# Kernel optimization log

Measured on AMD Instinct MI355X. Metric: run time of the kernel, lower is better.

Reference implementation:

```python
import jax, jax.numpy as jnp
import numpy as np

N_NODES = 100000
D = 64


def sage_conv(x, src, dst, W_l, b_l, W_r, n_nodes):
    """PyG SAGEConv with mean aggregation and root_weight=True:
    out_i = lin_l(mean_{j in N(i)} x_j) + lin_r(x_i)
    Aggregation happens on raw features (as in PyG), then linear transforms.
    """
    deg = jax.ops.segment_sum(jnp.ones_like(dst, dtype=x.dtype), dst, num_segments=n_nodes)
    aggr = jax.ops.segment_sum(x[src], dst, num_segments=n_nodes)  # [N, D] gather-scatter
    aggr = aggr / jnp.maximum(deg, 1.0)[:, None]                    # mean (0 for isolated nodes)
    return aggr @ W_l.T + b_l + x @ W_r.T


def setup_inputs() -> dict:
    key = jax.random.key(0)
    k_x, k_e, k1, k2, k3, k4 = jax.random.split(key, 6)
    x = jax.random.normal(k_x, (N_NODES, D), dtype=jnp.float32)
    edge_index = jax.random.randint(k_e, (2, 1600000), 0, N_NODES, dtype=jnp.int64)
    s = 1.0 / np.sqrt(D)
    # layer 1 (SAGEConv: lin_l has bias, lin_r has no bias)
    W1_l = jax.random.uniform(k1, (D, D), jnp.float32, -s, s)
    b1_l = jnp.zeros((D,), jnp.float32)
    W1_r = jax.random.uniform(k2, (D, D), jnp.float32, -s, s)
    # layer 2
    W2_l = jax.random.uniform(k3, (D, D), jnp.float32, -s, s)
    b2_l = jnp.zeros((D,), jnp.float32)
    W2_r = jax.random.uniform(k4, (D, D), jnp.float32, -s, s)
    return {"x": x, "edge_index": edge_index,
            "W1_l": W1_l, "b1_l": b1_l, "W1_r": W1_r,
            "W2_l": W2_l, "b2_l": b2_l, "W2_r": W2_r}


def reference(x, edge_index, W1_l, b1_l, W1_r, W2_l, b2_l, W2_r):
    src, dst = edge_index[0], edge_index[1]
    n = x.shape[0]
    x1 = sage_conv(x, src, dst, W1_l, b1_l, W1_r, n)
    x2 = sage_conv(x1, src, dst, W2_l, b2_l, W2_r, n)
    return x2
```

## Files before the change

kernel.cpp:

```cpp
#include <hip/hip_runtime.h>

#define DD 64
#define DTILE 128
#define BSHIFT 7
#define NBUCK_MAX 800
#define SEGCAP 4096

typedef unsigned short ushort_t;

static __device__ __forceinline__ unsigned short f2bf(float f)
{
    unsigned u = __float_as_uint(f);
    unsigned r = (u + 0x7FFFu + ((u >> 16) & 1u)) >> 16;
    return (unsigned short)r;
}
static __device__ __forceinline__ float bf_lo(unsigned w) { return __uint_as_float(w << 16); }
static __device__ __forceinline__ float bf_hi(unsigned w) { return __uint_as_float(w & 0xFFFF0000u); }


__global__ __launch_bounds__(256)
void bucket_count(const int* __restrict__ dst, int* __restrict__ partialCnt,
                  int nE, int chunk, int nbuck)
{
    __shared__ int bins[NBUCK_MAX];
    int blk = blockIdx.x, t = threadIdx.x;
    for (int i = t; i < nbuck; i += 256) bins[i] = 0;
    __syncthreads();
    int e0 = blk * chunk;
    int e1 = e0 + chunk; if (e1 > nE) e1 = nE;
    for (int e = e0 + t; e < e1; e += 256)
        atomicAdd(&bins[dst[e] >> BSHIFT], 1);
    __syncthreads();
    for (int i = t; i < nbuck; i += 256)
        partialCnt[(size_t)i * 256 + blk] = bins[i];
}

__global__ __launch_bounds__(256)
void bucket_scanblocks(int* __restrict__ partialCnt, int* __restrict__ bucketTot)
{
    __shared__ int s[256];
    int b = blockIdx.x, t = threadIdx.x;
    int v = partialCnt[(size_t)b * 256 + t];
    s[t] = v;
    __syncthreads();
    for (int off = 1; off < 256; off <<= 1) {
        int u = (t >= off) ? s[t - off] : 0;
        __syncthreads();
        s[t] += u;
        __syncthreads();
    }
    partialCnt[(size_t)b * 256 + t] = s[t] - v;
    if (t == 255) bucketTot[b] = s[255];
}

__global__ __launch_bounds__(1024)
void bucket_scanbase(const int* __restrict__ bucketTot, int* __restrict__ bucketBase,
                     int* __restrict__ rs, int nbuck, int nN)
{
    __shared__ int s[1024];
    int t = threadIdx.x;
    int v = (t < nbuck) ? bucketTot[t] : 0;
    s[t] = v;
    __syncthreads();
    for (int off = 1; off < 1024; off <<= 1) {
        int u = (t >= off) ? s[t - off] : 0;
        __syncthreads();
        s[t] += u;
        __syncthreads();
    }
    if (t < nbuck) bucketBase[t] = s[t] - v;
    if (t == nbuck - 1) {
        bucketBase[nbuck] = s[t];
        rs[nN] = s[t];
    }
}

__global__ __launch_bounds__(256)
void bucket_scatter(const int* __restrict__ src, const int* __restrict__ dst,
                    const int* __restrict__ partialCnt,
                    const int* __restrict__ bucketBase,
                    int* __restrict__ buckEdges, int nE, int chunk, int nbuck)
{
    __shared__ int bins[NBUCK_MAX];
    __shared__ int wOff[NBUCK_MAX];
    int blk = blockIdx.x, t = threadIdx.x;
    for (int i = t; i < nbuck; i += 256) {
        bins[i] = 0;
        wOff[i] = bucketBase[i] + partialCnt[(size_t)i * 256 + blk];
    }
    __syncthreads();
    int e0 = blk * chunk;
    int e1 = e0 + chunk; if (e1 > nE) e1 = nE;
    for (int e = e0 + t; e < e1; e += 256) {
        int d = dst[e];
        int sv = src[e];
        int bb = d >> BSHIFT;
        int r = atomicAdd(&bins[bb], 1);
        buckEdges[wOff[bb] + r] = sv | ((d & 127) << 17);
    }
}

__global__ __launch_bounds__(256)
void bucket_finalize(const int* __restrict__ buckEdges,
                     const int* __restrict__ bucketBase,
                     int* __restrict__ rs, int* __restrict__ csr,
                     int nN)
{
    __shared__ int eLds[SEGCAP];
    __shared__ int segLds[SEGCAP];
    __shared__ int deg[128];
    __shared__ int basec[128];
    __shared__ int cur[128];
    int b = blockIdx.x, t = threadIdx.x;
    int e0 = bucketBase[b], e1 = bucketBase[b + 1];
    int nb = e1 - e0;
    bool staged = (nb <= SEGCAP);
    if (t < 128) deg[t] = 0;
    __syncthreads();
    for (int i = t; i < nb; i += 256) {
        int p = buckEdges[e0 + i];
        if (staged) eLds[i] = p;
        atomicAdd(&deg[(p >> 17) & 127], 1);
    }
    __syncthreads();
    if (t < 128) basec[t] = deg[t];
    __syncthreads();
    for (int off = 1; off < 128; off <<= 1) {
        int u = 0;
        if (t < 128 && t >= off) u = basec[t - off];
        __syncthreads();
        if (t < 128) basec[t] += u;
        __syncthreads();
    }
    int nodeBase = b << BSHIFT;
    if (t < 128) {
        int node = nodeBase + t;
        int ex = basec[t] - deg[t];
        if (node < nN) rs[node] = e0 + ex;
        cur[t] = ex;
    }
    __syncthreads();
    for (int i = t; i < nb; i += 256) {
        int p = staged ? eLds[i] : buckEdges[e0 + i];
        int dl = (p >> 17) & 127;
        int slot = atomicAdd(&cur[dl], 1);
        int sv = p & 0x1FFFF;
        if (staged) segLds[slot] = sv;
        else        csr[e0 + slot] = sv;
    }
    __syncthreads();
    if (staged)
        for (int i = t; i < nb; i += 256)
            csr[e0 + i] = segLds[i];
}

__global__ __launch_bounds__(256)
void tobf16_kernel(const float* __restrict__ in, ushort_t* __restrict__ outh,
                   int nTot8)
{
    int i = blockIdx.x * 256 + threadIdx.x;
    if (i >= nTot8) return;
    float4 v0 = *(const float4*)(in + (size_t)i * 8);
    float4 v1 = *(const float4*)(in + (size_t)i * 8 + 4);
    uint4 o;
    o.x = (unsigned)f2bf(v0.x) | ((unsigned)f2bf(v0.y) << 16);
    o.y = (unsigned)f2bf(v0.z) | ((unsigned)f2bf(v0.w) << 16);
    o.z = (unsigned)f2bf(v1.x) | ((unsigned)f2bf(v1.y) << 16);
    o.w = (unsigned)f2bf(v1.z) | ((unsigned)f2bf(v1.w) << 16);
    *(uint4*)(outh + (size_t)i * 8) = o;
}

__global__ void prep_kernel(const float* __restrict__ W1l,
                            const float* __restrict__ W1r,
                            const float* __restrict__ W2l,
                            const float* __restrict__ W2r,
                            const float* __restrict__ b1,
                            const float* __restrict__ b2,
                            float* __restrict__ MT1, float* __restrict__ MT2,
                            float* __restrict__ MT3, float* __restrict__ c0,
                            float* __restrict__ c1)
{
    int f = blockIdx.x;
    int k = threadIdx.x;
    float m1 = 0.f, m2 = 0.f, m3 = 0.f;
    for (int j = 0; j < DD; ++j) {
        float a2l = W2l[f * DD + j];
        float a2r = W2r[f * DD + j];
        float w1l = W1l[j * DD + k];
        float w1r = W1r[j * DD + k];
        m1 = fmaf(a2l, w1l, m1);
        m2 = fmaf(a2l, w1r, m2);
        m2 = fmaf(a2r, w1l, m2);
        m3 = fmaf(a2r, w1r, m3);
    }
    MT1[k * DD + f] = m1;
    MT2[k * DD + f] = m2;
    MT3[k * DD + f] = m3;
    float t1 = W2l[f * DD + k] * b1[k];
    float t0 = W2r[f * DD + k] * b1[k];
    for (int off = 1; off < 64; off <<= 1) {
        t1 += __shfl_xor(t1, off);
        t0 += __shfl_xor(t0, off);
    }
    if (k == 0) {
        c1[f] = t1;
        c0[f] = t0 + b2[f];
    }
}

__global__ __launch_bounds__(256, 4)
void aggregate_bf16g(const ushort_t* __restrict__ xh,
                     const int* __restrict__ csr,
                     const int* __restrict__ rs,
                     ushort_t* __restrict__ aggrh, int nN)
{
    int lane = threadIdx.x & 63;
    int w = threadIdx.x >> 6;
    int g  = lane >> 3;
    int gl = lane & 7;
    int node = (blockIdx.x * 4 + w) * 8 + g;
    int valid = node < nN;
    int nd = valid ? node : nN - 1;
    int beg = rs[nd], end = rs[nd + 1];
    int deg = end - beg;

    float4 aL0 = {0,0,0,0}, aH0 = {0,0,0,0};
    float4 aL1 = {0,0,0,0}, aH1 = {0,0,0,0};
    float4 aL2 = {0,0,0,0}, aH2 = {0,0,0,0};
    float4 aL3 = {0,0,0,0}, aH3 = {0,0,0,0};

#define ROWA(S, L, H)                                                         \
    {                                                                         \
        uint4 v = *(const uint4*)(xh + (size_t)(S) * DD + gl * 8);            \
        L.x += bf_lo(v.x); L.y += bf_hi(v.x);                                 \
        L.z += bf_lo(v.y); L.w += bf_hi(v.y);                                 \
        H.x += bf_lo(v.z); H.y += bf_hi(v.z);                                 \
        H.z += bf_lo(v.w); H.w += bf_hi(v.w);                                 \
    }
#define ROWM(S, MM, L, H)                                                     \
    {                                                                         \
        uint4 v = *(const uint4*)(xh + (size_t)(S) * DD + gl * 8);            \
        L.x = fmaf(MM, bf_lo(v.x), L.x); L.y = fmaf(MM, bf_hi(v.x), L.y);     \
        L.z = fmaf(MM, bf_lo(v.y), L.z); L.w = fmaf(MM, bf_hi(v.y), L.w);     \
        H.x = fmaf(MM, bf_lo(v.z), H.x); H.y = fmaf(MM, bf_hi(v.z), H.y);     \
        H.z = fmaf(MM, bf_lo(v.w), H.z); H.w = fmaf(MM, bf_hi(v.w), H.w);     \
    }

    for (int ch = 0; ch < deg; ch += 8) {
        int ii = ch + gl;
        int myIdx = csr[(ii < deg) ? (beg + ii) : beg];
        int lb = g << 3;
        if (ch + 8 <= deg) {
            int s0 = __shfl(myIdx, lb + 0);
            int s1 = __shfl(myIdx, lb + 1);
            int s2 = __shfl(myIdx, lb + 2);
            int s3 = __shfl(myIdx, lb + 3);
            ROWA(s0, aL0, aH0) ROWA(s1, aL1, aH1)
            ROWA(s2, aL2, aH2) ROWA(s3, aL3, aH3)
            int s4 = __shfl(myIdx, lb + 4);
            int s5 = __shfl(myIdx, lb + 5);
            int s6 = __shfl(myIdx, lb + 6);
            int s7 = __shfl(myIdx, lb + 7);
            ROWA(s4, aL0, aH0) ROWA(s5, aL1, aH1)
            ROWA(s6, aL2, aH2) ROWA(s7, aL3, aH3)
        } else {
            int rem = deg - ch;
            int s0 = __shfl(myIdx, lb + 0);
            int s1 = __shfl(myIdx, lb + 1);
            int s2 = __shfl(myIdx, lb + 2);
            int s3 = __shfl(myIdx, lb + 3);
            float m0 = (0 < rem) ? 1.f : 0.f;
            float m1 = (1 < rem) ? 1.f : 0.f;
            float m2 = (2 < rem) ? 1.f : 0.f;
            float m3 = (3 < rem) ? 1.f : 0.f;
            ROWM(s0, m0, aL0, aH0) ROWM(s1, m1, aL1, aH1)
            ROWM(s2, m2, aL2, aH2) ROWM(s3, m3, aL3, aH3)
            int s4 = __shfl(myIdx, lb + 4);
            int s5 = __shfl(myIdx, lb + 5);
            int s6 = __shfl(myIdx, lb + 6);
            int s7 = __shfl(myIdx, lb + 7);
            float m4 = (4 < rem) ? 1.f : 0.f;
            float m5 = (5 < rem) ? 1.f : 0.f;
            float m6 = (6 < rem) ? 1.f : 0.f;
            float m7 = (7 < rem) ? 1.f : 0.f;
            ROWM(s4, m4, aL0, aH0) ROWM(s5, m5, aL1, aH1)
            ROWM(s6, m6, aL2, aH2) ROWM(s7, m7, aL3, aH3)
        }
    }
#undef ROWA
#undef ROWM

    float4 L, H;
    L.x = (aL0.x + aL1.x) + (aL2.x + aL3.x);
    L.y = (aL0.y + aL1.y) + (aL2.y + aL3.y);
    L.z = (aL0.z + aL1.z) + (aL2.z + aL3.z);
    L.w = (aL0.w + aL1.w) + (aL2.w + aL3.w);
    H.x = (aH0.x + aH1.x) + (aH2.x + aH3.x);
    H.y = (aH0.y + aH1.y) + (aH2.y + aH3.y);
    H.z = (aH0.z + aH1.z) + (aH2.z + aH3.z);
    H.w = (aH0.w + aH1.w) + (aH2.w + aH3.w);
    if (valid) {
        float inv = 1.0f / (float)(deg > 0 ? deg : 1);
        uint4 o;
        o.x = (unsigned)f2bf(L.x * inv) | ((unsigned)f2bf(L.y * inv) << 16);
        o.y = (unsigned)f2bf(L.z * inv) | ((unsigned)f2bf(L.w * inv) << 16);
        o.z = (unsigned)f2bf(H.x * inv) | ((unsigned)f2bf(H.y * inv) << 16);
        o.w = (unsigned)f2bf(H.z * inv) | ((unsigned)f2bf(H.w * inv) << 16);
        *(uint4*)(aggrh + (size_t)node * DD + gl * 8) = o;
    }
}

__global__ __launch_bounds__(512)
void tri_dense6(const ushort_t* __restrict__ agg2h,
                const ushort_t* __restrict__ agg1h,
                const ushort_t* __restrict__ xh,
                const float* __restrict__ MT1,
                const float* __restrict__ MT2,
                const float* __restrict__ MT3,
                const float* __restrict__ c0,
                const float* __restrict__ c1,
                const int* __restrict__ rs,
                float* __restrict__ out, int nN)
{
    __shared__ float t_lds[DTILE * 65];
    int tid = threadIdx.x;
    int nl  = tid & 127;
    int fbase = __builtin_amdgcn_readfirstlane((tid >> 7) * 16);
    int base = blockIdx.x * DTILE;
    int node = base + nl;
    int gn = node < nN ? node : nN - 1;

    float ind = (rs[gn + 1] - rs[gn]) > 0 ? 1.0f : 0.0f;
    float acc[16];
#pragma unroll
    for (int j = 0; j < 16; ++j)
        acc[j] = fmaf(ind, c1[fbase + j], c0[fbase + j]);

#define STAGE(SRCH)                                                           \
    {                                                                         \
        _Pragma("unroll")                                                     \
        for (int i = 0; i < 2; ++i) {                                         \
            int fi = i * 512 + tid;                  \
            int row = fi >> 3;                                                \
            int col = (fi & 7) * 8;                                           \
            int grow = base + row;                                            \
            if (grow >= nN) grow = nN - 1;                                    \
            uint4 v = *(const uint4*)((SRCH) + (size_t)grow * DD + col);      \
            float4 lo, hi;                                                    \
            lo.x = bf_lo(v.x); lo.y = bf_hi(v.x);                             \
            lo.z = bf_lo(v.y); lo.w = bf_hi(v.y);                             \
            hi.x = bf_lo(v.z); hi.y = bf_hi(v.z);                             \
            hi.z = bf_lo(v.w); hi.w = bf_hi(v.w);                             \
            *(float4*)&t_lds[row * 65 + col] = lo;                            \
            *(float4*)&t_lds[row * 65 + col + 4] = hi;                        \
        }                                                                     \
    }

#define PHASE(MT)                                                             \
    {                                                                         \
        _Pragma("unroll 1")                                                   \
        for (int k = 0; k < DD; k += 4) {                                     \
            float i0 = t_lds[nl * 65 + k + 0];                                \
            float i1 = t_lds[nl * 65 + k + 1];                                \
            float i2 = t_lds[nl * 65 + k + 2];                                \
            float i3 = t_lds[nl * 65 + k + 3];                                \
            const float* mr = (MT) + k * DD + fbase;                          \
            _Pragma("unroll")                                                 \
            for (int j = 0; j < 16; ++j) acc[j] = fmaf(i0, mr[j], acc[j]);    \
            _Pragma("unroll")                                                 \
            for (int j = 0; j < 16; ++j) acc[j] = fmaf(i1, mr[DD + j], acc[j]); \
            _Pragma("unroll")                                                 \
            for (int j = 0; j < 16; ++j) acc[j] = fmaf(i2, mr[2 * DD + j], acc[j]); \
            _Pragma("unroll")                                                 \
            for (int j = 0; j < 16; ++j) acc[j] = fmaf(i3, mr[3 * DD + j], acc[j]); \
        }                                                                     \
    }

    STAGE(agg2h);
    __syncthreads();
    PHASE(MT1);
    __syncthreads();
    STAGE(agg1h);
    __syncthreads();
    PHASE(MT2);
    __syncthreads();
    STAGE(xh);
    __syncthreads();
    PHASE(MT3);
    __syncthreads();

#pragma unroll
    for (int j = 0; j < 16; j += 4) {
        float4 o;
        o.x = acc[j]; o.y = acc[j + 1]; o.z = acc[j + 2]; o.w = acc[j + 3];
        *(float4*)&t_lds[nl * 65 + fbase + j] = o;
    }
    __syncthreads();
#pragma unroll
    for (int i = 0; i < 4; ++i) {
        int fi = i * 512 + tid;
        int row = fi >> 4;
        int col = (fi & 15) * 4;
        int grow = base + row;
        if (grow < nN)
            *(float4*)(out + (size_t)grow * DD + col) = *(float4*)&t_lds[row * 65 + col];
    }
#undef STAGE
#undef PHASE
}

extern "C" void kernel_launch(void* const* d_in, const int* in_sizes, int n_in,
                              void* d_out, int out_size, void* d_ws, size_t ws_size,
                              hipStream_t stream)
{
    const float* x   = (const float*)d_in[0];
    const int*   ei  = (const int*)d_in[1];
    const float* W1l = (const float*)d_in[2];
    const float* b1l = (const float*)d_in[3];
    const float* W1r = (const float*)d_in[4];
    const float* W2l = (const float*)d_in[5];
    const float* b2l = (const float*)d_in[6];
    const float* W2r = (const float*)d_in[7];
    float* out = (float*)d_out;

    int nN = in_sizes[0] / DD;
    int nE = in_sizes[1] / 2;
    const int* src = ei;
    const int* dst = ei + nE;

    int nbuck = (nN + 127) >> BSHIFT;
    int chunk = (nE + 255) / 256;

    int* rs         = (int*)d_ws;
    int* partialCnt = rs + nN + 1;
    int* bucketTot  = partialCnt + (size_t)nbuck * 256;
    int* bucketBase = bucketTot + nbuck;
    int* csr        = bucketBase + nbuck + 1;
    int* buckEdges  = csr + nE;
    size_t ofs = (size_t)(buckEdges + nE - (int*)d_ws);
    ofs = (ofs + 3) & ~(size_t)3;
    float* MT1 = (float*)d_ws + ofs;
    float* MT2 = MT1 + DD * DD;
    float* MT3 = MT2 + DD * DD;
    float* c0 = MT3 + DD * DD;
    float* c1 = c0 + DD;
    float* xh_f    = c1 + DD;
    float* agg1h_f = xh_f + (size_t)nN * 32;
    float* agg2h_f = agg1h_f + (size_t)nN * 32;
    ushort_t* xh    = (ushort_t*)xh_f;
    ushort_t* agg1h = (ushort_t*)agg1h_f;
    ushort_t* agg2h = (ushort_t*)agg2h_f;

    int nden = (nN + DTILE - 1) / DTILE;
    int ncv  = (nN * 32 / 4 + 255) / 256;
    int nagg = (nN + 31) / 32;

    bucket_count<<<256, 256, 0, stream>>>(dst, partialCnt, nE, chunk, nbuck);
    bucket_scanblocks<<<nbuck, 256, 0, stream>>>(partialCnt, bucketTot);
    bucket_scanbase<<<1, 1024, 0, stream>>>(bucketTot, bucketBase, rs, nbuck, nN);
    bucket_scatter<<<256, 256, 0, stream>>>(src, dst, partialCnt, bucketBase,
                                            buckEdges, nE, chunk, nbuck);
    bucket_finalize<<<nbuck, 256, 0, stream>>>(buckEdges, bucketBase, rs, csr, nN);

    prep_kernel<<<64, 64, 0, stream>>>(W1l, W1r, W2l, W2r, b1l, b2l,
                                       MT1, MT2, MT3, c0, c1);
    tobf16_kernel<<<ncv, 256, 0, stream>>>(x, xh, nN * DD / 8);

    aggregate_bf16g<<<nagg, 256, 0, stream>>>(xh, csr, rs, agg1h, nN);
    aggregate_bf16g<<<nagg, 256, 0, stream>>>(agg1h, csr, rs, agg2h, nN);

    tri_dense6<<<nden, 512, 0, stream>>>(agg2h, agg1h, xh, MT1, MT2, MT3,
                                         c0, c1, rs, out, nN);
}
```

Before: 159.3 us.

## Replace fused dense epilogue with bf16 MFMA kernel and prepacked weights

```diff
diff --git a/kernel.cpp b/kernel.cpp
--- a/kernel.cpp
+++ b/kernel.cpp
@@ -1,12 +1,14 @@
 #include <hip/hip_runtime.h>
 
 #define DD 64
-#define DTILE 128
 #define BSHIFT 7
 #define NBUCK_MAX 800
 #define SEGCAP 4096
 
 typedef unsigned short ushort_t;
+typedef __attribute__((ext_vector_type(8))) short bf16x8;
+typedef __attribute__((ext_vector_type(4))) short bf16x4;
+typedef __attribute__((ext_vector_type(4))) float f32x4;
 
 static __device__ __forceinline__ unsigned short f2bf(float f)
 {
@@ -104,7 +106,7 @@
 void bucket_finalize(const int* __restrict__ buckEdges,
                      const int* __restrict__ bucketBase,
                      int* __restrict__ rs, int* __restrict__ csr,
-                     int nN)
+                     float* __restrict__ indf, int nN)
 {
     __shared__ int eLds[SEGCAP];
     __shared__ int segLds[SEGCAP];
@@ -136,7 +138,10 @@
     if (t < 128) {
         int node = nodeBase + t;
         int ex = basec[t] - deg[t];
-        if (node < nN) rs[node] = e0 + ex;
+        if (node < nN) {
+            rs[node] = e0 + ex;
+            indf[node] = deg[t] > 0 ? 1.0f : 0.0f;
+        }
         cur[t] = ex;
     }
     __syncthreads();
@@ -206,6 +211,24 @@
         c1[f] = t1;
         c0[f] = t0 + b2[f];
     }
+}
+
+__global__ __launch_bounds__(256)
+void pack_weights(const float* __restrict__ MT1, const float* __restrict__ MT2,
+                  const float* __restrict__ MT3, ushort_t* __restrict__ Wp)
+{
+    int idx = blockIdx.x * 256 + threadIdx.x;
+    if (idx >= 12288) return;
+    int e    = idx & 7;
+    int lane = (idx >> 3) & 63;
+    int ft   = (idx >> 9) & 3;
+    int kt   = (idx >> 11) & 1;
+    int m    = idx >> 12;
+    int kin  = ((lane >> 4) * 4) + (e & 3) + 16 * (e >> 2);
+    int gk   = kt * 32 + kin;
+    int f    = ft * 16 + (lane & 15);
+    const float* MT = (m == 0) ? MT1 : (m == 1) ? MT2 : MT3;
+    Wp[idx] = f2bf(MT[gk * DD + f]);
 }
 
 __global__ __launch_bounds__(256, 4)
@@ -310,103 +333,66 @@
     }
 }
 
-__global__ __launch_bounds__(512)
-void tri_dense6(const ushort_t* __restrict__ agg2h,
-                const ushort_t* __restrict__ agg1h,
-                const ushort_t* __restrict__ xh,
-                const float* __restrict__ MT1,
-                const float* __restrict__ MT2,
-                const float* __restrict__ MT3,
-                const float* __restrict__ c0,
-                const float* __restrict__ c1,
-                const int* __restrict__ rs,
-                float* __restrict__ out, int nN)
-{
-    __shared__ float t_lds[DTILE * 65];
-    int tid = threadIdx.x;
-    int nl  = tid & 127;
-    int fbase = __builtin_amdgcn_readfirstlane((tid >> 7) * 16);
-    int base = blockIdx.x * DTILE;
-    int node = base + nl;
-    int gn = node < nN ? node : nN - 1;
-
-    float ind = (rs[gn + 1] - rs[gn]) > 0 ? 1.0f : 0.0f;
-    float acc[16];
-#pragma unroll
-    for (int j = 0; j < 16; ++j)
-        acc[j] = fmaf(ind, c1[fbase + j], c0[fbase + j]);
-
-#define STAGE(SRCH)                                                           \
+__global__ __launch_bounds__(256)
+void tri_dense_mfma(const ushort_t* __restrict__ agg2h,
+                    const ushort_t* __restrict__ agg1h,
+                    const ushort_t* __restrict__ xh,
+                    const ushort_t* __restrict__ Wp,
+                    const float* __restrict__ c0,
+                    const float* __restrict__ c1,
+                    const float* __restrict__ indf,
+                    float* __restrict__ out, int nN)
+{
+    int lane = threadIdx.x & 63;
+    int w = threadIdx.x >> 6;
+    int base = (blockIdx.x * 4 + w) * 16;
+    if (base >= nN) return;
+    int mrow = lane & 15;
+    int kg   = lane >> 4;
+    f32x4 acc0 = {0,0,0,0}, acc1 = {0,0,0,0}, acc2 = {0,0,0,0}, acc3 = {0,0,0,0};
+
+#define DO_SRC(S, m)                                                          \
     {                                                                         \
+        const ushort_t* rowp = (S) + (size_t)(base + mrow) * DD + kg * 4;     \
         _Pragma("unroll")                                                     \
-        for (int i = 0; i < 2; ++i) {                                         \
-            int fi = i * 512 + tid;                  \
-            int row = fi >> 3;                                                \
-            int col = (fi & 7) * 8;                                           \
-            int grow = base + row;                                            \
-            if (grow >= nN) grow = nN - 1;                                    \
-            uint4 v = *(const uint4*)((SRCH) + (size_t)grow * DD + col);      \
-            float4 lo, hi;                                                    \
-            lo.x = bf_lo(v.x); lo.y = bf_hi(v.x);                             \
-            lo.z = bf_lo(v.y); lo.w = bf_hi(v.y);                             \
-            hi.x = bf_lo(v.z); hi.y = bf_hi(v.z);                             \
-            hi.z = bf_lo(v.w); hi.w = bf_hi(v.w);                             \
-            *(float4*)&t_lds[row * 65 + col] = lo;                            \
-            *(float4*)&t_lds[row * 65 + col + 4] = hi;                        \
+        for (int kt = 0; kt < 2; ++kt) {                                      \
+            bf16x4 lo = *(const bf16x4*)(rowp + kt * 32);                     \
+            bf16x4 hi = *(const bf16x4*)(rowp + kt * 32 + 16);                \
+            bf16x8 a;                                                         \
+            a[0] = lo[0]; a[1] = lo[1]; a[2] = lo[2]; a[3] = lo[3];           \
+            a[4] = hi[0]; a[5] = hi[1]; a[6] = hi[2]; a[7] = hi[3];           \
+            const ushort_t* wp = Wp + (((m) * 2 + kt) * 4) * 512 + lane * 8;  \
+            bf16x8 b0 = *(const bf16x8*)(wp);                                 \
+            bf16x8 b1 = *(const bf16x8*)(wp + 512);                           \
+            bf16x8 b2 = *(const bf16x8*)(wp + 1024);                          \
+            bf16x8 b3 = *(const bf16x8*)(wp + 1536);                          \
+            acc0 = __builtin_amdgcn_mfma_f32_16x16x32_bf16(a, b0, acc0, 0, 0, 0); \
+            acc1 = __builtin_amdgcn_mfma_f32_16x16x32_bf16(a, b1, acc1, 0, 0, 0); \
+            acc2 = __builtin_amdgcn_mfma_f32_16x16x32_bf16(a, b2, acc2, 0, 0, 0); \
+            acc3 = __builtin_amdgcn_mfma_f32_16x16x32_bf16(a, b3, acc3, 0, 0, 0); \
         }                                                                     \
     }
-
-#define PHASE(MT)                                                             \
+    DO_SRC(agg2h, 0)
+    DO_SRC(agg1h, 1)
+    DO_SRC(xh,    2)
+#undef DO_SRC
+
+    float ind0 = indf[base + kg * 4 + 0];
+    float ind1 = indf[base + kg * 4 + 1];
+    float ind2 = indf[base + kg * 4 + 2];
+    float ind3 = indf[base + kg * 4 + 3];
+#define STORE_T(ACC, ft)                                                      \
     {                                                                         \
-        _Pragma("unroll 1")                                                   \
-        for (int k = 0; k < DD; k += 4) {                                     \
-            float i0 = t_lds[nl * 65 + k + 0];                                \
-            float i1 = t_lds[nl * 65 + k + 1];                                \
-            float i2 = t_lds[nl * 65 + k + 2];                                \
-            float i3 = t_lds[nl * 65 + k + 3];                                \
-            const float* mr = (MT) + k * DD + fbase;                          \
-            _Pragma("unroll")                                                 \
-            for (int j = 0; j < 16; ++j) acc[j] = fmaf(i0, mr[j], acc[j]);    \
-            _Pragma("unroll")                                                 \
-            for (int j = 0; j < 16; ++j) acc[j] = fmaf(i1, mr[DD + j], acc[j]); \
-            _Pragma("unroll")                                                 \
-            for (int j = 0; j < 16; ++j) acc[j] = fmaf(i2, mr[2 * DD + j], acc[j]); \
-            _Pragma("unroll")                                                 \
-            for (int j = 0; j < 16; ++j) acc[j] = fmaf(i3, mr[3 * DD + j], acc[j]); \
-        }                                                                     \
-    }
-
-    STAGE(agg2h);
-    __syncthreads();
-    PHASE(MT1);
-    __syncthreads();
-    STAGE(agg1h);
-    __syncthreads();
-    PHASE(MT2);
-    __syncthreads();
-    STAGE(xh);
-    __syncthreads();
-    PHASE(MT3);
-    __syncthreads();
-
-#pragma unroll
-    for (int j = 0; j < 16; j += 4) {
-        float4 o;
-        o.x = acc[j]; o.y = acc[j + 1]; o.z = acc[j + 2]; o.w = acc[j + 3];
-        *(float4*)&t_lds[nl * 65 + fbase + j] = o;
-    }
-    __syncthreads();
-#pragma unroll
-    for (int i = 0; i < 4; ++i) {
-        int fi = i * 512 + tid;
-        int row = fi >> 4;
-        int col = (fi & 15) * 4;
-        int grow = base + row;
-        if (grow < nN)
-            *(float4*)(out + (size_t)grow * DD + col) = *(float4*)&t_lds[row * 65 + col];
-    }
-#undef STAGE
-#undef PHASE
+        int f = (ft) * 16 + mrow;                                             \
+        float b0v = c0[f], b1v = c1[f];                                       \
+        size_t o = (size_t)(base + kg * 4) * DD + f;                          \
+        out[o         ] = ACC[0] + b0v + ind0 * b1v;                          \
+        out[o + DD    ] = ACC[1] + b0v + ind1 * b1v;                          \
+        out[o + 2 * DD] = ACC[2] + b0v + ind2 * b1v;                          \
+        out[o + 3 * DD] = ACC[3] + b0v + ind3 * b1v;                          \
+    }
+    STORE_T(acc0, 0) STORE_T(acc1, 1) STORE_T(acc2, 2) STORE_T(acc3, 3)
+#undef STORE_T
 }
 
 extern "C" void kernel_launch(void* const* d_in, const int* in_sizes, int n_in,
@@ -447,28 +433,32 @@
     float* xh_f    = c1 + DD;
     float* agg1h_f = xh_f + (size_t)nN * 32;
     float* agg2h_f = agg1h_f + (size_t)nN * 32;
+    float* indf    = agg2h_f + (size_t)nN * 32;
+    ushort_t* Wp   = (ushort_t*)(indf + nN);
     ushort_t* xh    = (ushort_t*)xh_f;
     ushort_t* agg1h = (ushort_t*)agg1h_f;
     ushort_t* agg2h = (ushort_t*)agg2h_f;
 
-    int nden = (nN + DTILE - 1) / DTILE;
     int ncv  = (nN * 32 / 4 + 255) / 256;
     int nagg = (nN + 31) / 32;
+    int nmf  = (nN / 16 + 3) / 4;
 
     bucket_count<<<256, 256, 0, stream>>>(dst, partialCnt, nE, chunk, nbuck);
     bucket_scanblocks<<<nbuck, 256, 0, stream>>>(partialCnt, bucketTot);
     bucket_scanbase<<<1, 1024, 0, stream>>>(bucketTot, bucketBase, rs, nbuck, nN);
     bucket_scatter<<<256, 256, 0, stream>>>(src, dst, partialCnt, bucketBase,
                                             buckEdges, nE, chunk, nbuck);
-    bucket_finalize<<<nbuck, 256, 0, stream>>>(buckEdges, bucketBase, rs, csr, nN);
+    bucket_finalize<<<nbuck, 256, 0, stream>>>(buckEdges, bucketBase, rs, csr,
+                                               indf, nN);
 
     prep_kernel<<<64, 64, 0, stream>>>(W1l, W1r, W2l, W2r, b1l, b2l,
                                        MT1, MT2, MT3, c0, c1);
+    pack_weights<<<48, 256, 0, stream>>>(MT1, MT2, MT3, Wp);
     tobf16_kernel<<<ncv, 256, 0, stream>>>(x, xh, nN * DD / 8);
 
     aggregate_bf16g<<<nagg, 256, 0, stream>>>(xh, csr, rs, agg1h, nN);
     aggregate_bf16g<<<nagg, 256, 0, stream>>>(agg1h, csr, rs, agg2h, nN);
 
-    tri_dense6<<<nden, 512, 0, stream>>>(agg2h, agg1h, xh, MT1, MT2, MT3,
-                                         c0, c1, rs, out, nN);
-}
+    tri_dense_mfma<<<nmf, 256, 0, stream>>>(agg2h, agg1h, xh, Wp,
+                                            c0, c1, indf, out, nN);
+}
```

Result: faster. 140.2 us (-12.0%).
